# Optimization experiments

Measured on AMD Instinct MI355X. Metric: run time of the kernel, lower is better.

The kernel has to match this reference:

```python
import jax, jax.numpy as jnp
import numpy as np

N, E, DN, DE, H = 50000, 800000, 64, 64, 128


def setup_inputs() -> dict:
    key = jax.random.key(0)
    ks = jax.random.split(key, 12)
    s = 0.05
    return {
        "h": jax.random.normal(ks[0], (N, DN), jnp.float32),
        "eh": jax.random.normal(ks[1], (E, DE), jnp.float32),
        "W_node1": jax.random.normal(ks[2], (DN, H), jnp.float32) * s,
        "b_node1": jax.random.normal(ks[3], (H,), jnp.float32) * s,
        "W_node2": jax.random.normal(ks[4], (H, H), jnp.float32) * s,
        "W_edge1": jax.random.normal(ks[5], (DE, H), jnp.float32) * s,
        "b_edge1": jax.random.normal(ks[6], (H,), jnp.float32) * s,
        "W_edge2": jax.random.normal(ks[7], (H, H), jnp.float32) * s,
        "W_comb": jax.random.normal(ks[8], (H, DN), jnp.float32) * s,
        "W_ue": jax.random.normal(ks[9], (DN, DE), jnp.float32) * s,
        "src": jax.random.randint(ks[10], (E,), 0, N, jnp.int32),
        "dst": jax.random.randint(ks[11], (E,), 0, N, jnp.int32),
    }


def reference(h, eh, W_node1, b_node1, W_node2, W_edge1, b_edge1, W_edge2, W_comb, W_ue, src, dst):
    # gather per-edge endpoint node features: [E, DN]
    hs = h[src]
    hd = h[dst]
    # edge update: h_e = 0.8*h_e + 0.2 * fc_update_edge(h_src * h_dst)
    eh_new = 0.8 * eh + 0.2 * ((hs * hd) @ W_ue)
    # message: two small MLPs then tanh-combine, all per edge
    m1 = jax.nn.relu(hs @ W_node1 + b_node1) @ W_node2       # [E, H]
    m2 = jax.nn.relu(eh_new @ W_edge1 + b_edge1) @ W_edge2   # [E, H]
    m = jnp.tanh((m1 * m2) @ W_comb)                          # [E, DN]
    # reduce: scatter-sum messages to destination nodes + residual
    agg = jax.ops.segment_sum(m, dst, num_segments=h.shape[0])
    return agg + h
```

## Files before the change

kernel.cpp:

```cpp
#include <hip/hip_runtime.h>
#include <hip/hip_bf16.h>

#define NN 50000
#define NE 800000
#define DNODE 64
#define HD 128

typedef __attribute__((ext_vector_type(8)))  short bf16x8;
typedef __attribute__((ext_vector_type(16))) float f32x16;
typedef __attribute__((ext_vector_type(4)))  float f32x4;
typedef __attribute__((ext_vector_type(4)))  unsigned short u16x4;
typedef __attribute__((ext_vector_type(8)))  unsigned short u16x8;

__device__ __forceinline__ short f2bf(float f) {
    __hip_bfloat16 b = __float2bfloat16(f);
    unsigned short u;
    __builtin_memcpy(&u, &b, 2);
    return (short)u;
}
__device__ __forceinline__ float bf2f(unsigned short s) {
    return __uint_as_float(((unsigned)s) << 16);
}
__device__ __forceinline__ f32x16 zero16() {
    f32x16 z;
#pragma unroll
    for (int i = 0; i < 16; ++i) z[i] = 0.f;
    return z;
}

__device__ __forceinline__ unsigned cvt_pk(float lo, float hi) {
    unsigned r;
    asm("v_cvt_pk_bf16_f32 %0, %1, %2" : "=v"(r) : "v"(lo), "v"(hi));
    return r;
}

__device__ __forceinline__ void atomic_pk_bf16(unsigned short* addr, unsigned data) {
    unsigned long long a = (unsigned long long)(uintptr_t)addr;
    asm volatile("global_atomic_pk_add_bf16 %0, %1, off" :: "v"(a), "v"(data) : "memory");
}

__device__ __forceinline__ bf16x8 pack_swap(const float* v) {
    unsigned w0 = cvt_pk(v[0], v[1]);
    unsigned w1 = cvt_pk(v[2], v[3]);
    unsigned w2 = cvt_pk(v[4], v[5]);
    unsigned w3 = cvt_pk(v[6], v[7]);
    asm("v_permlane32_swap_b32 %0, %1" : "+v"(w0), "+v"(w2));
    asm("v_permlane32_swap_b32 %0, %1" : "+v"(w1), "+v"(w3));
    union { unsigned u[4]; bf16x8 f; } o;
    o.u[0] = w0; o.u[1] = w1; o.u[2] = w2; o.u[3] = w3;
    return o.f;
}

__device__ __forceinline__ void build_frags(const float* __restrict__ W, int ncols,
                                            int nks, int nct, bf16x8* dst,
                                            int tid, int nthr) {
    int total = nct * nks * 64;
    for (int p = tid; p < total; p += nthr) {
        int fi = p >> 6, l = p & 63;
        int ct = fi / nks, ks = fi - ct * nks;
        int col = 32 * ct + (l & 31);
        int kb  = 16 * ks + 8 * (l >> 5);
        bf16x8 v;
#pragma unroll
        for (int j = 0; j < 8; ++j) v[j] = f2bf(W[(size_t)(kb + j) * ncols + col]);
        dst[p] = v;
    }
}

__global__ __launch_bounds__(512, 4) void node_kernel(
        const float* __restrict__ h, const float* __restrict__ Wn1,
        const float* __restrict__ bn1, const float* __restrict__ Wn2,
        unsigned short* __restrict__ M1, int ntiles) {
    __shared__ bf16x8 fWn1[16 * 64];
    __shared__ bf16x8 fWn2[32 * 64];
    __shared__ float  bias[HD];

    int tid = threadIdx.x;
    build_frags(Wn1, HD, 4, 4, fWn1, tid, 512);
    build_frags(Wn2, HD, 8, 4, fWn2, tid, 512);
    if (tid < HD) bias[tid] = bn1[tid];
    __syncthreads();

    int wv = tid >> 6, lane = tid & 63;
    int la = lane & 31, hh = lane >> 5;

    int tile = blockIdx.x * 8 + wv;
    if (tile >= ntiles) return;
    int n0 = tile * 32;
    int n_la = n0 + la;
    int nc = n_la < NN ? n_la : NN - 1;

    bf16x8 hfrag[4];
#pragma unroll
    for (int ks = 0; ks < 4; ++ks) {
        int cb = 16 * ks + 8 * hh;
        f32x4 h0 = *(const f32x4*)&h[(size_t)nc * DNODE + cb];
        f32x4 h1 = *(const f32x4*)&h[(size_t)nc * DNODE + cb + 4];
        union { unsigned u[4]; bf16x8 f; } xf;
        xf.u[0] = cvt_pk(h0[0], h0[1]);
        xf.u[1] = cvt_pk(h0[2], h0[3]);
        xf.u[2] = cvt_pk(h1[0], h1[1]);
        xf.u[3] = cvt_pk(h1[2], h1[3]);
        hfrag[ks] = xf.f;
    }

    bf16x8 tfrag[8];
#pragma unroll
    for (int ct = 0; ct < 4; ++ct) {
        f32x16 acc = zero16();
#pragma unroll
        for (int ks = 0; ks < 4; ++ks)
            acc = __builtin_amdgcn_mfma_f32_32x32x16_bf16(fWn1[(ct * 4 + ks) * 64 + lane], hfrag[ks], acc, 0, 0, 0);
        float vals[16];
#pragma unroll
        for (int m = 0; m < 4; ++m) {
            f32x4 bv = *(const f32x4*)&bias[32 * ct + 8 * m + 4 * hh];
#pragma unroll
            for (int j = 0; j < 4; ++j)
                vals[4 * m + j] = fmaxf(acc[4 * m + j] + bv[j], 0.f);
        }
        tfrag[2 * ct]     = pack_swap(&vals[0]);
        tfrag[2 * ct + 1] = pack_swap(&vals[8]);
    }

#pragma unroll
    for (int ct = 0; ct < 4; ++ct) {
        f32x16 acc = zero16();
#pragma unroll
        for (int ks = 0; ks < 8; ++ks)
            acc = __builtin_amdgcn_mfma_f32_32x32x16_bf16(tfrag[ks], fWn2[(ct * 8 + ks) * 64 + lane], acc, 0, 0, 0);
#pragma unroll
        for (int r = 0; r < 16; ++r) {
            int row = (r & 3) + 8 * (r >> 2) + 4 * hh;
            int node = n0 + row;
            if (node < NN)
                M1[(size_t)node * HD + 32 * ct + la] = (unsigned short)f2bf(acc[r]);
        }
    }
}

__global__ __launch_bounds__(512, 4) void edge_kernel(
        const float* __restrict__ h, const float* __restrict__ eh,
        const float* __restrict__ Wue, const float* __restrict__ We1,
        const float* __restrict__ be1, const float* __restrict__ We2,
        const float* __restrict__ Wcb, const int* __restrict__ src,
        const int* __restrict__ dst, const unsigned short* __restrict__ M1,
        unsigned short* __restrict__ Macc) {
    __shared__ bf16x8 fUe[8 * 64];
    __shared__ bf16x8 fE1[16 * 64];
    __shared__ bf16x8 fE2[32 * 64];
    __shared__ bf16x8 fCb[16 * 64];
    __shared__ float  bias[HD];

    int tid = threadIdx.x;
    build_frags(Wue, 64, 4, 2, fUe, tid, 512);
    build_frags(We1, HD, 4, 4, fE1, tid, 512);
    build_frags(We2, HD, 8, 4, fE2, tid, 512);
    build_frags(Wcb, 64, 8, 2, fCb, tid, 512);
    if (tid < HD) bias[tid] = be1[tid];
    __syncthreads();

    int wv = tid >> 6, lane = tid & 63;
    int la = lane & 31, hh = lane >> 5;

    const int NT = NE / 32;
    int gw = blockIdx.x * 8 + wv;
    int t0 = (int)(((long long)gw * NT) >> 12);
    int t1 = (int)(((long long)(gw + 1) * NT) >> 12);
    if (t0 >= t1) return;

    int srcA = src[t0 * 32 + la];
    int dstA = dst[t0 * 32 + la];

    for (int t = t0; t < t1; ++t) {
        int e_la = t * 32 + la;
        int eN = (t + 1 < t1) ? (t + 1) * 32 + la : e_la;
        int srcN = src[eN];
        int dstN = dst[eN];

        u16x4 mq[16];
#pragma unroll
        for (int ct = 0; ct < 4; ++ct)
#pragma unroll
            for (int m = 0; m < 4; ++m)
                mq[4 * ct + m] = *(const u16x4*)&M1[(size_t)srcA * HD + 32 * ct + 8 * m + 4 * hh];
        f32x4 ehq[8];
#pragma unroll
        for (int ct = 0; ct < 2; ++ct)
#pragma unroll
            for (int m = 0; m < 4; ++m)
                ehq[4 * ct + m] = *(const f32x4*)&eh[(size_t)e_la * 64 + 32 * ct + 8 * m + 4 * hh];

        f32x16 accU0 = zero16(), accU1 = zero16();
#pragma unroll
        for (int ks = 0; ks < 4; ++ks) {
            int cb = 16 * ks + 8 * hh;
            f32x4 s0 = *(const f32x4*)&h[(size_t)srcA * DNODE + cb];
            f32x4 s1 = *(const f32x4*)&h[(size_t)srcA * DNODE + cb + 4];
            f32x4 d0 = *(const f32x4*)&h[(size_t)dstA * DNODE + cb];
            f32x4 d1 = *(const f32x4*)&h[(size_t)dstA * DNODE + cb + 4];
            union { unsigned u[4]; bf16x8 f; } xf;
            xf.u[0] = cvt_pk(s0[0] * d0[0], s0[1] * d0[1]);
            xf.u[1] = cvt_pk(s0[2] * d0[2], s0[3] * d0[3]);
            xf.u[2] = cvt_pk(s1[0] * d1[0], s1[1] * d1[1]);
            xf.u[3] = cvt_pk(s1[2] * d1[2], s1[3] * d1[3]);
            accU0 = __builtin_amdgcn_mfma_f32_32x32x16_bf16(fUe[(0 * 4 + ks) * 64 + lane], xf.f, accU0, 0, 0, 0);
            accU1 = __builtin_amdgcn_mfma_f32_32x32x16_bf16(fUe[(1 * 4 + ks) * 64 + lane], xf.f, accU1, 0, 0, 0);
        }

        bf16x8 efrag[4];
#pragma unroll
        for (int ct = 0; ct < 2; ++ct) {
            const f32x16& aU = ct ? accU1 : accU0;
            float vals[16];
#pragma unroll
            for (int m = 0; m < 4; ++m)
#pragma unroll
                for (int j = 0; j < 4; ++j)
                    vals[4 * m + j] = 0.8f * ehq[4 * ct + m][j] + 0.2f * aU[4 * m + j];
            efrag[2 * ct]     = pack_swap(&vals[0]);
            efrag[2 * ct + 1] = pack_swap(&vals[8]);
        }

        bf16x8 tfrag[8];
#pragma unroll
        for (int ct = 0; ct < 4; ++ct) {
            f32x16 acc = zero16();
#pragma unroll
            for (int ks = 0; ks < 4; ++ks)
                acc = __builtin_amdgcn_mfma_f32_32x32x16_bf16(fE1[(ct * 4 + ks) * 64 + lane], efrag[ks], acc, 0, 0, 0);
            float vals[16];
#pragma unroll
            for (int m = 0; m < 4; ++m) {
                f32x4 bv = *(const f32x4*)&bias[32 * ct + 8 * m + 4 * hh];
#pragma unroll
                for (int j = 0; j < 4; ++j)
                    vals[4 * m + j] = fmaxf(acc[4 * m + j] + bv[j], 0.f);
            }
            tfrag[2 * ct]     = pack_swap(&vals[0]);
            tfrag[2 * ct + 1] = pack_swap(&vals[8]);
        }

        bf16x8 pfrag[8];
#pragma unroll
        for (int ct = 0; ct < 4; ++ct) {
            f32x16 acc = zero16();
#pragma unroll
            for (int ks = 0; ks < 8; ++ks)
                acc = __builtin_amdgcn_mfma_f32_32x32x16_bf16(fE2[(ct * 8 + ks) * 64 + lane], tfrag[ks], acc, 0, 0, 0);
            float vals[16];
#pragma unroll
            for (int m = 0; m < 4; ++m)
#pragma unroll
                for (int j = 0; j < 4; ++j)
                    vals[4 * m + j] = acc[4 * m + j] * bf2f(mq[4 * ct + m][j]);
            pfrag[2 * ct]     = pack_swap(&vals[0]);
            pfrag[2 * ct + 1] = pack_swap(&vals[8]);
        }

        int dstR[16];
#pragma unroll
        for (int r = 0; r < 16; ++r)
            dstR[r] = __shfl(dstA, (r & 3) + 8 * (r >> 2) + 4 * hh);

        f32x16 accF0 = zero16(), accF1 = zero16();
#pragma unroll
        for (int ks = 0; ks < 8; ++ks) {
            accF0 = __builtin_amdgcn_mfma_f32_32x32x16_bf16(pfrag[ks], fCb[(0 * 8 + ks) * 64 + lane], accF0, 0, 0, 0);
            accF1 = __builtin_amdgcn_mfma_f32_32x32x16_bf16(pfrag[ks], fCb[(1 * 8 + ks) * 64 + lane], accF1, 0, 0, 0);
        }
        int odd = lane & 1;
#pragma unroll
        for (int r = 0; r < 16; ++r) {
            float x0 = fminf(fmaxf(accF0[r], -10.f), 10.f);
            float x1 = fminf(fmaxf(accF1[r], -10.f), 10.f);
            float ex0 = __expf(2.f * x0), ex1 = __expf(2.f * x1);
            float m0 = (ex0 - 1.f) * __builtin_amdgcn_rcpf(ex0 + 1.f);
            float m1 = (ex1 - 1.f) * __builtin_amdgcn_rcpf(ex1 + 1.f);
            float e0 = __shfl_xor(m0, 1);
            float e1 = __shfl_xor(m1, 1);
            unsigned w = odd ? cvt_pk(e1, m1) : cvt_pk(m0, e0);
            int colstart = odd ? (31 + la) : la;
            atomic_pk_bf16(&Macc[(size_t)dstR[r] * 64 + colstart], w);
        }

        srcA = srcN;
        dstA = dstN;
    }
}

__global__ __launch_bounds__(256) void combine_kernel(
        const float* __restrict__ h, const unsigned short* __restrict__ Macc,
        float* __restrict__ out) {
    int i = (blockIdx.x * 256 + threadIdx.x) * 8;
    if (i >= NN * DNODE) return;
    u16x8 mv = *(const u16x8*)&Macc[i];
    f32x4 h0 = *(const f32x4*)&h[i];
    f32x4 h1 = *(const f32x4*)&h[i + 4];
    f32x4 o0, o1;
#pragma unroll
    for (int j = 0; j < 4; ++j) {
        o0[j] = h0[j] + bf2f(mv[j]);
        o1[j] = h1[j] + bf2f(mv[4 + j]);
    }
    *(f32x4*)&out[i]     = o0;
    *(f32x4*)&out[i + 4] = o1;
}

extern "C" void kernel_launch(void* const* d_in, const int* in_sizes, int n_in,
                              void* d_out, int out_size, void* d_ws, size_t ws_size,
                              hipStream_t stream) {
    const float* h   = (const float*)d_in[0];
    const float* eh  = (const float*)d_in[1];
    const float* Wn1 = (const float*)d_in[2];
    const float* bn1 = (const float*)d_in[3];
    const float* Wn2 = (const float*)d_in[4];
    const float* We1 = (const float*)d_in[5];
    const float* be1 = (const float*)d_in[6];
    const float* We2 = (const float*)d_in[7];
    const float* Wcb = (const float*)d_in[8];
    const float* Wue = (const float*)d_in[9];
    const int*   src = (const int*)d_in[10];
    const int*   dst = (const int*)d_in[11];
    float* out = (float*)d_out;

    unsigned short* M1   = (unsigned short*)d_ws;
    unsigned short* Macc = (unsigned short*)((char*)d_ws + (size_t)NN * HD * 2);

    hipMemsetAsync(Macc, 0, (size_t)NN * DNODE * 2, stream);
    int ntiles = (NN + 31) / 32;
    node_kernel<<<(ntiles + 7) / 8, 512, 0, stream>>>(h, Wn1, bn1, Wn2, M1, ntiles);
    edge_kernel<<<512, 512, 0, stream>>>(h, eh, Wue, We1, be1, We2, Wcb, src, dst, M1, Macc);
    combine_kernel<<<(NN * DNODE / 8 + 255) / 256, 256, 0, stream>>>(h, Macc, out);
}
```

Baseline: 478.0 us.

## Gather bf16 node features, prefetch next tile's gathers, permute M1 layout

The node kernel now writes a bf16 copy of h, and the edge kernel gathers src/dst rows from it instead of from fp32 h, halving gather bytes. Those gathers are software-pipelined one tile ahead, with indices loaded two tiles ahead. M1 is stored in a permuted layout so each lane reads its 128-byte slice with wide contiguous loads. The edge launch changes to 256 blocks of 768 threads. Rounding h to bf16 before the product slightly changes numerics, and the extra prefetch registers may pressure occupancy.

```diff
diff --git a/kernel.cpp b/kernel.cpp
--- a/kernel.cpp
+++ b/kernel.cpp
@@ -70,7 +70,8 @@
 __global__ __launch_bounds__(512, 4) void node_kernel(
         const float* __restrict__ h, const float* __restrict__ Wn1,
         const float* __restrict__ bn1, const float* __restrict__ Wn2,
-        unsigned short* __restrict__ M1, int ntiles) {
+        unsigned short* __restrict__ M1, unsigned short* __restrict__ hb16,
+        int ntiles) {
     __shared__ bf16x8 fWn1[16 * 64];
     __shared__ bf16x8 fWn2[32 * 64];
     __shared__ float  bias[HD];
@@ -96,12 +97,14 @@
         int cb = 16 * ks + 8 * hh;
         f32x4 h0 = *(const f32x4*)&h[(size_t)nc * DNODE + cb];
         f32x4 h1 = *(const f32x4*)&h[(size_t)nc * DNODE + cb + 4];
-        union { unsigned u[4]; bf16x8 f; } xf;
+        union { unsigned u[4]; bf16x8 f; u16x8 s; } xf;
         xf.u[0] = cvt_pk(h0[0], h0[1]);
         xf.u[1] = cvt_pk(h0[2], h0[3]);
         xf.u[2] = cvt_pk(h1[0], h1[1]);
         xf.u[3] = cvt_pk(h1[2], h1[3]);
         hfrag[ks] = xf.f;
+        if (n_la < NN)
+            *(u16x8*)((char*)hb16 + (size_t)n_la * 128 + 32 * ks + 16 * hh) = xf.s;
     }
 
     bf16x8 tfrag[8];
@@ -123,6 +126,7 @@
         tfrag[2 * ct + 1] = pack_swap(&vals[8]);
     }
 
+    int moff = ((la >> 2) & 1) * 64 + (la >> 3) * 4 + (la & 3);
 #pragma unroll
     for (int ct = 0; ct < 4; ++ct) {
         f32x16 acc = zero16();
@@ -134,13 +138,13 @@
             int row = (r & 3) + 8 * (r >> 2) + 4 * hh;
             int node = n0 + row;
             if (node < NN)
-                M1[(size_t)node * HD + 32 * ct + la] = (unsigned short)f2bf(acc[r]);
-        }
-    }
-}
-
-__global__ __launch_bounds__(512, 4) void edge_kernel(
-        const float* __restrict__ h, const float* __restrict__ eh,
+                M1[(size_t)node * HD + moff + ct * 16] = (unsigned short)f2bf(acc[r]);
+        }
+    }
+}
+
+__global__ __launch_bounds__(768, 3) void edge_kernel(
+        const unsigned short* __restrict__ hb16, const float* __restrict__ eh,
         const float* __restrict__ Wue, const float* __restrict__ We1,
         const float* __restrict__ be1, const float* __restrict__ We2,
         const float* __restrict__ Wcb, const int* __restrict__ src,
@@ -153,10 +157,10 @@
     __shared__ float  bias[HD];
 
     int tid = threadIdx.x;
-    build_frags(Wue, 64, 4, 2, fUe, tid, 512);
-    build_frags(We1, HD, 4, 4, fE1, tid, 512);
-    build_frags(We2, HD, 8, 4, fE2, tid, 512);
-    build_frags(Wcb, 64, 8, 2, fCb, tid, 512);
+    build_frags(Wue, 64, 4, 2, fUe, tid, 768);
+    build_frags(We1, HD, 4, 4, fE1, tid, 768);
+    build_frags(We2, HD, 8, 4, fE2, tid, 768);
+    build_frags(Wcb, 64, 8, 2, fCb, tid, 768);
     if (tid < HD) bias[tid] = be1[tid];
     __syncthreads();
 
@@ -164,46 +168,51 @@
     int la = lane & 31, hh = lane >> 5;
 
     const int NT = NE / 32;
-    int gw = blockIdx.x * 8 + wv;
-    int t0 = (int)(((long long)gw * NT) >> 12);
-    int t1 = (int)(((long long)(gw + 1) * NT) >> 12);
+    const int NW = 3072;
+    int gw = blockIdx.x * 12 + wv;
+    int t0 = (int)(((long long)gw * NT) / NW);
+    int t1 = (int)(((long long)(gw + 1) * NT) / NW);
     if (t0 >= t1) return;
 
-    int srcA = src[t0 * 32 + la];
-    int dstA = dst[t0 * 32 + la];
+    const char* hb = (const char*)hb16;
+
+    int srcA = src[t0 * 32 + la], dstA = dst[t0 * 32 + la];
+    int tB = (t0 + 1 < t1) ? t0 + 1 : t0;
+    int srcB = src[tB * 32 + la], dstB = dst[tB * 32 + la];
+    u16x8 hsA[4], hdA[4];
+#pragma unroll
+    for (int ks = 0; ks < 4; ++ks) {
+        hsA[ks] = *(const u16x8*)(hb + (size_t)srcA * 128 + 32 * ks + 16 * hh);
+        hdA[ks] = *(const u16x8*)(hb + (size_t)dstA * 128 + 32 * ks + 16 * hh);
+    }
 
     for (int t = t0; t < t1; ++t) {
         int e_la = t * 32 + la;
-        int eN = (t + 1 < t1) ? (t + 1) * 32 + la : e_la;
-        int srcN = src[eN];
-        int dstN = dst[eN];
-
-        u16x4 mq[16];
-#pragma unroll
-        for (int ct = 0; ct < 4; ++ct)
-#pragma unroll
-            for (int m = 0; m < 4; ++m)
-                mq[4 * ct + m] = *(const u16x4*)&M1[(size_t)srcA * HD + 32 * ct + 8 * m + 4 * hh];
+
+        u16x8 mqv[8];
+        const char* m1b = (const char*)M1 + (size_t)srcA * 256 + hh * 128;
+#pragma unroll
+        for (int q = 0; q < 8; ++q)
+            mqv[q] = *(const u16x8*)(m1b + 16 * q);
         f32x4 ehq[8];
 #pragma unroll
         for (int ct = 0; ct < 2; ++ct)
 #pragma unroll
             for (int m = 0; m < 4; ++m)
                 ehq[4 * ct + m] = *(const f32x4*)&eh[(size_t)e_la * 64 + 32 * ct + 8 * m + 4 * hh];
+        int tC = (t + 2 < t1) ? t + 2 : t1 - 1;
+        int srcC = src[tC * 32 + la], dstC = dst[tC * 32 + la];
 
         f32x16 accU0 = zero16(), accU1 = zero16();
 #pragma unroll
         for (int ks = 0; ks < 4; ++ks) {
-            int cb = 16 * ks + 8 * hh;
-            f32x4 s0 = *(const f32x4*)&h[(size_t)srcA * DNODE + cb];
-            f32x4 s1 = *(const f32x4*)&h[(size_t)srcA * DNODE + cb + 4];
-            f32x4 d0 = *(const f32x4*)&h[(size_t)dstA * DNODE + cb];
-            f32x4 d1 = *(const f32x4*)&h[(size_t)dstA * DNODE + cb + 4];
             union { unsigned u[4]; bf16x8 f; } xf;
-            xf.u[0] = cvt_pk(s0[0] * d0[0], s0[1] * d0[1]);
-            xf.u[1] = cvt_pk(s0[2] * d0[2], s0[3] * d0[3]);
-            xf.u[2] = cvt_pk(s1[0] * d1[0], s1[1] * d1[1]);
-            xf.u[3] = cvt_pk(s1[2] * d1[2], s1[3] * d1[3]);
+#pragma unroll
+            for (int i = 0; i < 4; ++i) {
+                float a0 = bf2f(hsA[ks][2 * i])     * bf2f(hdA[ks][2 * i]);
+                float a1 = bf2f(hsA[ks][2 * i + 1]) * bf2f(hdA[ks][2 * i + 1]);
+                xf.u[i] = cvt_pk(a0, a1);
+            }
             accU0 = __builtin_amdgcn_mfma_f32_32x32x16_bf16(fUe[(0 * 4 + ks) * 64 + lane], xf.f, accU0, 0, 0, 0);
             accU1 = __builtin_amdgcn_mfma_f32_32x32x16_bf16(fUe[(1 * 4 + ks) * 64 + lane], xf.f, accU1, 0, 0, 0);
         }
@@ -220,6 +229,12 @@
                     vals[4 * m + j] = 0.8f * ehq[4 * ct + m][j] + 0.2f * aU[4 * m + j];
             efrag[2 * ct]     = pack_swap(&vals[0]);
             efrag[2 * ct + 1] = pack_swap(&vals[8]);
+        }
+
+#pragma unroll
+        for (int ks = 0; ks < 4; ++ks) {
+            hsA[ks] = *(const u16x8*)(hb + (size_t)srcB * 128 + 32 * ks + 16 * hh);
+            hdA[ks] = *(const u16x8*)(hb + (size_t)dstB * 128 + 32 * ks + 16 * hh);
         }
 
         bf16x8 tfrag[8];
@@ -250,10 +265,12 @@
                 acc = __builtin_amdgcn_mfma_f32_32x32x16_bf16(fE2[(ct * 8 + ks) * 64 + lane], tfrag[ks], acc, 0, 0, 0);
             float vals[16];
 #pragma unroll
-            for (int m = 0; m < 4; ++m)
+            for (int m = 0; m < 4; ++m) {
+                u16x8 Q = mqv[2 * ct + (m >> 1)];
 #pragma unroll
                 for (int j = 0; j < 4; ++j)
-                    vals[4 * m + j] = acc[4 * m + j] * bf2f(mq[4 * ct + m][j]);
+                    vals[4 * m + j] = acc[4 * m + j] * bf2f(Q[(m & 1) * 4 + j]);
+            }
             pfrag[2 * ct]     = pack_swap(&vals[0]);
             pfrag[2 * ct + 1] = pack_swap(&vals[8]);
         }
@@ -284,8 +301,7 @@
             atomic_pk_bf16(&Macc[(size_t)dstR[r] * 64 + colstart], w);
         }
 
-        srcA = srcN;
-        dstA = dstN;
+        srcA = srcB; dstA = dstB; srcB = srcC; dstB = dstC;
     }
 }
 
@@ -326,10 +342,11 @@
 
     unsigned short* M1   = (unsigned short*)d_ws;
     unsigned short* Macc = (unsigned short*)((char*)d_ws + (size_t)NN * HD * 2);
+    unsigned short* hb16 = (unsigned short*)((char*)d_ws + (size_t)NN * (HD + DNODE) * 2);
 
     hipMemsetAsync(Macc, 0, (size_t)NN * DNODE * 2, stream);
     int ntiles = (NN + 31) / 32;
-    node_kernel<<<(ntiles + 7) / 8, 512, 0, stream>>>(h, Wn1, bn1, Wn2, M1, ntiles);
-    edge_kernel<<<512, 512, 0, stream>>>(h, eh, Wue, We1, be1, We2, Wcb, src, dst, M1, Macc);
+    node_kernel<<<(ntiles + 7) / 8, 512, 0, stream>>>(h, Wn1, bn1, Wn2, M1, hb16, ntiles);
+    edge_kernel<<<256, 768, 0, stream>>>(hb16, eh, Wue, We1, be1, We2, Wcb, src, dst, M1, Macc);
     combine_kernel<<<(NN * DNODE / 8 + 255) / 256, 256, 0, stream>>>(h, Macc, out);
 }
```

After: 431.4 us. -9.8%, faster.
